# Kernel optimization log

Hardware: AMD Instinct MI355X
Metric: run time of the kernel (lower is better)

Reference implementation:

```python
import jax, jax.numpy as jnp
import numpy as np

NEG = -1000000000.0

def setup_inputs() -> dict:
    key = jax.random.key(0)
    kq, kk, kv, km = jax.random.split(key, 4)
    B, H, S, D = 2, 4, 4096, 64
    q = jax.random.normal(kq, (B, H, S, D), dtype=jnp.float32)
    k = jax.random.normal(kk, (B, H, S, D), dtype=jnp.float32)
    v = jax.random.normal(kv, (B, H, S, D), dtype=jnp.float32)
    mask = jax.random.randint(km, (1, S, S), 0, 2, dtype=jnp.int32)
    return {"q": q, "k": k, "v": v, "mask": mask}

def reference(q, k, v, mask):
    # scores: [B,H,S,S]
    attn = jnp.einsum('bhsd,bhtd->bhst', q, k)
    attn = attn / jnp.sqrt(jnp.asarray(k.shape[-1], dtype=jnp.float32))
    # torch cat/view just broadcasts mask [1,S,S] to [B,H,S,S]
    m = jnp.broadcast_to(mask.astype(bool)[:, None, :, :], attn.shape)
    attn = jnp.where(m, jnp.float32(NEG), attn)
    # NOTE: original module uses nn.Softmax(dim=0) -> softmax over batch axis
    attn = jax.nn.softmax(attn, axis=0)
    out = jnp.einsum('bhst,bhtd->bhsd', attn, v)
    return (out, attn)
```

## Files before the change

kernel.cpp:

```cpp
#include <hip/hip_runtime.h>

#define SDIM 4096
#define DDIM 64
#define HDIM 4
#define OUTN (2 * HDIM * SDIM * DDIM)
#define NTZ 4

typedef short short8 __attribute__((ext_vector_type(8)));
typedef short bh4    __attribute__((ext_vector_type(4)));
typedef float f32x4  __attribute__((ext_vector_type(4)));

__device__ inline short f2bf(float f) {
    unsigned u = __builtin_bit_cast(unsigned, f);
    u = (u + 0x7fffu + ((u >> 16) & 1u)) >> 16;
    return (short)u;
}
__device__ inline float bf2f(short s) {
    unsigned u = ((unsigned)(unsigned short)s) << 16;
    return __builtin_bit_cast(float, u);
}

__device__ inline short* ldsp(short* base, int row, int colshort) {
    int byte = (row << 7) + (colshort << 1);
    byte ^= (row & 7) << 4;
    return (short*)((char*)base + byte);
}

__device__ inline void g2l16(const short* g, short* l) {
    __builtin_amdgcn_global_load_lds(
        (const __attribute__((address_space(1))) unsigned int*)g,
        (__attribute__((address_space(3))) unsigned int*)l, 16, 0, 0);
}

__global__ void pack_mask(const int* __restrict__ mask,
                          unsigned long long* __restrict__ bits) {
    int gid = blockIdx.x * 256 + threadIdx.x;
    int v = (mask[gid] != 0);
    unsigned long long bal = __ballot(v);
    if ((threadIdx.x & 63) == 0) bits[gid >> 6] = bal;
}

__global__ void cvt_bf16(const float* __restrict__ src, short* __restrict__ dst) {
    int gid = blockIdx.x * 256 + threadIdx.x;
    const float* p = src + (size_t)gid * 8;
    f32x4 a = *(const f32x4*)p;
    f32x4 b = *(const f32x4*)(p + 4);
    short8 o;
#pragma unroll
    for (int j = 0; j < 4; ++j) { o[j] = f2bf(a[j]); o[j + 4] = f2bf(b[j]); }
    *(short8*)(dst + (size_t)gid * 8) = o;
}

__global__ void transpose_v(const float* __restrict__ v, short* __restrict__ vt) {
    int gid = blockIdx.x * 256 + threadIdx.x;
    int t8 = gid & (SDIM / 8 - 1);
    int d  = (gid >> 9) & (DDIM - 1);
    int bh = gid >> 15;
    short8 o;
#pragma unroll
    for (int j = 0; j < 8; ++j)
        o[j] = f2bf(v[((size_t)bh * SDIM + t8 * 8 + j) * DDIM + d]);
    *(short8*)(vt + ((size_t)bh * DDIM + d) * SDIM + t8 * 8) = o;
}

__global__ __launch_bounds__(256, 3)
void attn_fused(const short* __restrict__ qg, const short* __restrict__ kg,
                const short* __restrict__ vtg,
                const unsigned long long* __restrict__ mbits,
                float* __restrict__ attng, float* __restrict__ outg,
                float* __restrict__ opart) {
    __shared__ short Ks [2][64 * 64];
    __shared__ short VTs[2][64 * 64];
    __shared__ short Ps [64 * 64];

    const int h   = blockIdx.y;
    const int s0  = blockIdx.x << 6;
    const int tz  = blockIdx.z;
    const int tid = threadIdx.x;
    const int wv  = tid >> 6;
    const int ln  = tid & 63;
    const int l   = ln & 15;
    const int qd  = ln >> 4;

    short8 qf[2][2];
#pragma unroll
    for (int b = 0; b < 2; ++b) {
        const size_t rb = ((size_t)(b * HDIM + h) * SDIM + (s0 + wv * 16 + l)) * DDIM;
#pragma unroll
        for (int kc = 0; kc < 2; ++kc)
            qf[b][kc] = *(const short8*)(qg + rb + kc * 32 + qd * 8);
    }

    f32x4 oacc[2][4];
#pragma unroll
    for (int b = 0; b < 2; ++b)
#pragma unroll
        for (int nd = 0; nd < 4; ++nd)
            oacc[b][nd] = (f32x4){0.f, 0.f, 0.f, 0.f};

    const int ln8 = ln >> 3;
    const int sc_ = (ln & 7) ^ ln8;
    const int mrow0 = s0 + wv * 16 + qd * 4;

    const int tbeg = tz * (SDIM / NTZ);
    for (int t0 = tbeg; t0 < tbeg + SDIM / NTZ; t0 += 64) {
        __syncthreads();
#pragma unroll
        for (int b = 0; b < 2; ++b) {
            const short* kb = kg  + ((size_t)(b * HDIM + h) * SDIM + t0) * DDIM;
            const short* vb = vtg + ((size_t)(b * HDIM + h) * DDIM) * SDIM + t0;
#pragma unroll
            for (int p = 0; p < 2; ++p) {
                int rr = p * 32 + wv * 8 + ln8;
                g2l16(kb + (size_t)rr * DDIM + sc_ * 8, &Ks [b][p * 2048 + wv * 512]);
                g2l16(vb + (size_t)rr * SDIM + sc_ * 8, &VTs[b][p * 2048 + wv * 512]);
            }
        }
        unsigned long long mw[4];
#pragma unroll
        for (int rg = 0; rg < 4; ++rg)
            mw[rg] = mbits[(size_t)(mrow0 + rg) * (SDIM / 64) + (t0 >> 6)];
        __syncthreads();

        f32x4 sc[2][4];
#pragma unroll
        for (int b = 0; b < 2; ++b)
#pragma unroll
            for (int nt = 0; nt < 4; ++nt) {
                f32x4 acc = (f32x4){0.f, 0.f, 0.f, 0.f};
#pragma unroll
                for (int kc = 0; kc < 2; ++kc) {
                    short8 bf = *(const short8*)ldsp(&Ks[b][0], nt * 16 + l, kc * 32 + qd * 8);
                    acc = __builtin_amdgcn_mfma_f32_16x16x32_bf16(qf[b][kc], bf, acc, 0, 0, 0);
                }
                sc[b][nt] = acc;
            }

#pragma unroll
        for (int nt = 0; nt < 4; ++nt)
#pragma unroll
            for (int rg = 0; rg < 4; ++rg) {
                float dd = (sc[0][nt][rg] - sc[1][nt][rg]) * 0.125f;
                bool msk = (mw[rg] >> (nt * 16 + l)) & 1ull;
                float p0 = msk ? 0.5f : __builtin_amdgcn_rcpf(1.f + __expf(-dd));
                int row = wv * 16 + qd * 4 + rg;
                *ldsp(&Ps[0], row, nt * 16 + l) = f2bf(p0);
            }

#pragma unroll
        for (int kc = 0; kc < 2; ++kc) {
            short8 af0 = *(const short8*)ldsp(&Ps[0], wv * 16 + l, kc * 32 + qd * 8);
            short8 af1;
#pragma unroll
            for (int j = 0; j < 8; ++j) af1[j] = f2bf(1.f - bf2f(af0[j]));
#pragma unroll
            for (int nd = 0; nd < 4; ++nd) {
                short8 bf = *(const short8*)ldsp(&VTs[0][0], nd * 16 + l, kc * 32 + qd * 8);
                oacc[0][nd] = __builtin_amdgcn_mfma_f32_16x16x32_bf16(af0, bf, oacc[0][nd], 0, 0, 0);
                short8 bf1 = *(const short8*)ldsp(&VTs[1][0], nd * 16 + l, kc * 32 + qd * 8);
                oacc[1][nd] = __builtin_amdgcn_mfma_f32_16x16x32_bf16(af1, bf1, oacc[1][nd], 0, 0, 0);
            }
        }

        {
            int rr2 = ln >> 4;
            int c2  = ln & 15;
            size_t ab0 = ((size_t)(0 * HDIM + h) * SDIM + s0) * (size_t)SDIM + t0;
            size_t ab1 = ((size_t)(1 * HDIM + h) * SDIM + s0) * (size_t)SDIM + t0;
#pragma unroll
            for (int sub = 0; sub < 4; ++sub) {
                int row = wv * 16 + sub * 4 + rr2;
                bh4 pv = *(const bh4*)ldsp(&Ps[0], row, c2 * 4);
                f32x4 o0, o1;
#pragma unroll
                for (int j = 0; j < 4; ++j) { o0[j] = bf2f(pv[j]); o1[j] = 1.f - o0[j]; }
                __builtin_nontemporal_store(
                    o0, (f32x4*)(attng + ab0 + (size_t)row * SDIM + c2 * 4));
                __builtin_nontemporal_store(
                    o1, (f32x4*)(attng + ab1 + (size_t)row * SDIM + c2 * 4));
            }
        }
    }

    float* dst = (tz == 0) ? outg : (opart + (size_t)(tz - 1) * OUTN);
#pragma unroll
    for (int b = 0; b < 2; ++b)
#pragma unroll
        for (int nd = 0; nd < 4; ++nd)
#pragma unroll
            for (int rg = 0; rg < 4; ++rg) {
                int srow = s0 + wv * 16 + qd * 4 + rg;
                dst[((size_t)(b * HDIM + h) * SDIM + srow) * DDIM + nd * 16 + l] =
                    oacc[b][nd][rg];
            }
}

__global__ void combine(const float* __restrict__ opart, float* __restrict__ outg) {
    int gid = blockIdx.x * 256 + threadIdx.x;
    f32x4 a = *(const f32x4*)(outg + (size_t)gid * 4);
#pragma unroll
    for (int s = 0; s < NTZ - 1; ++s)
        a = a + *(const f32x4*)(opart + (size_t)s * OUTN + (size_t)gid * 4);
    *(f32x4*)(outg + (size_t)gid * 4) = a;
}

extern "C" void kernel_launch(void* const* d_in, const int* in_sizes, int n_in,
                              void* d_out, int out_size, void* d_ws, size_t ws_size,
                              hipStream_t stream) {
    (void)in_sizes; (void)n_in; (void)out_size; (void)ws_size;
    const float* qg  = (const float*)d_in[0];
    const float* kg  = (const float*)d_in[1];
    const float* vg  = (const float*)d_in[2];
    const int*   msk = (const int*)d_in[3];

    float* outg  = (float*)d_out;
    float* attng = outg + (size_t)OUTN;

    char* ws = (char*)d_ws;
    unsigned long long* bits = (unsigned long long*)ws;
    short* qb = (short*)(ws + (size_t) 2 * 1024 * 1024);
    short* kb = (short*)(ws + (size_t) 6 * 1024 * 1024);
    short* vt = (short*)(ws + (size_t)10 * 1024 * 1024);
    float* op = (float*)(ws + (size_t)14 * 1024 * 1024);

    pack_mask  <<<dim3(SDIM * SDIM / 256), dim3(256), 0, stream>>>(msk, bits);
    cvt_bf16   <<<dim3(OUTN / (8 * 256)), dim3(256), 0, stream>>>(qg, qb);
    cvt_bf16   <<<dim3(OUTN / (8 * 256)), dim3(256), 0, stream>>>(kg, kb);
    transpose_v<<<dim3(OUTN / (8 * 256)), dim3(256), 0, stream>>>(vg, vt);
    attn_fused <<<dim3(SDIM / 64, HDIM, NTZ), dim3(256), 0, stream>>>(
        qb, kb, vt, bits, attng, outg, op);
    combine    <<<dim3(OUTN / (4 * 256)), dim3(256), 0, stream>>>(op, outg);
}
```

Before: 217.9 us.

## Compute transposed score tiles and store attention straight from registers in fp32

The QK^T MFMA now takes K as the A operand, so each lane holds four consecutive key columns of one query row. The attention probabilities can then be written to global memory directly from registers as f32x4 stores, with no round trip through the LDS Ps buffer. The mask bit layout is transposed to match, so each lane loads one 64-bit word per tile. The key-dimension split drops from 4 to 2, which lowers the partial-output traffic in combine, and launch bounds drop to 2 blocks per CU. The trade-off is fewer blocks in flight, and the per-lane attention stores are less coalesced, each row being split into 16-byte pieces per lane.

```diff
diff --git a/kernel.cpp b/kernel.cpp
--- a/kernel.cpp
+++ b/kernel.cpp
@@ -4,7 +4,6 @@
 #define DDIM 64
 #define HDIM 4
 #define OUTN (2 * HDIM * SDIM * DDIM)
-#define NTZ 4
 
 typedef short short8 __attribute__((ext_vector_type(8)));
 typedef short bh4    __attribute__((ext_vector_type(4)));
@@ -37,7 +36,11 @@
     int gid = blockIdx.x * 256 + threadIdx.x;
     int v = (mask[gid] != 0);
     unsigned long long bal = __ballot(v);
-    if ((threadIdx.x & 63) == 0) bits[gid >> 6] = bal;
+    if ((threadIdx.x & 63) == 0) {
+        int row = gid >> 12;
+        int tch = (gid & (SDIM - 1)) >> 6;
+        bits[(size_t)tch * SDIM + row] = bal;
+    }
 }
 
 __global__ void cvt_bf16(const float* __restrict__ src, short* __restrict__ dst) {
@@ -63,7 +66,7 @@
     *(short8*)(vt + ((size_t)bh * DDIM + d) * SDIM + t8 * 8) = o;
 }
 
-__global__ __launch_bounds__(256, 3)
+__global__ __launch_bounds__(256, 2)
 void attn_fused(const short* __restrict__ qg, const short* __restrict__ kg,
                 const short* __restrict__ vtg,
                 const unsigned long long* __restrict__ mbits,
@@ -100,10 +103,10 @@
 
     const int ln8 = ln >> 3;
     const int sc_ = (ln & 7) ^ ln8;
-    const int mrow0 = s0 + wv * 16 + qd * 4;
-
-    const int tbeg = tz * (SDIM / NTZ);
-    for (int t0 = tbeg; t0 < tbeg + SDIM / NTZ; t0 += 64) {
+    const int mrow = s0 + wv * 16 + l;
+
+    const int tbeg = tz * (SDIM / 2);
+    for (int t0 = tbeg; t0 < tbeg + SDIM / 2; t0 += 64) {
         __syncthreads();
 #pragma unroll
         for (int b = 0; b < 2; ++b) {
@@ -116,10 +119,7 @@
                 g2l16(vb + (size_t)rr * SDIM + sc_ * 8, &VTs[b][p * 2048 + wv * 512]);
             }
         }
-        unsigned long long mw[4];
-#pragma unroll
-        for (int rg = 0; rg < 4; ++rg)
-            mw[rg] = mbits[(size_t)(mrow0 + rg) * (SDIM / 64) + (t0 >> 6)];
+        unsigned long long mw = mbits[(size_t)(t0 >> 6) * SDIM + mrow];
         __syncthreads();
 
         f32x4 sc[2][4];
@@ -130,22 +130,39 @@
                 f32x4 acc = (f32x4){0.f, 0.f, 0.f, 0.f};
 #pragma unroll
                 for (int kc = 0; kc < 2; ++kc) {
-                    short8 bf = *(const short8*)ldsp(&Ks[b][0], nt * 16 + l, kc * 32 + qd * 8);
-                    acc = __builtin_amdgcn_mfma_f32_16x16x32_bf16(qf[b][kc], bf, acc, 0, 0, 0);
+                    short8 kf = *(const short8*)ldsp(&Ks[b][0], nt * 16 + l, kc * 32 + qd * 8);
+                    acc = __builtin_amdgcn_mfma_f32_16x16x32_bf16(kf, qf[b][kc], acc, 0, 0, 0);
                 }
                 sc[b][nt] = acc;
             }
 
-#pragma unroll
-        for (int nt = 0; nt < 4; ++nt)
+        f32x4 p0[4];
+#pragma unroll
+        for (int nt = 0; nt < 4; ++nt) {
 #pragma unroll
             for (int rg = 0; rg < 4; ++rg) {
                 float dd = (sc[0][nt][rg] - sc[1][nt][rg]) * 0.125f;
-                bool msk = (mw[rg] >> (nt * 16 + l)) & 1ull;
-                float p0 = msk ? 0.5f : __builtin_amdgcn_rcpf(1.f + __expf(-dd));
-                int row = wv * 16 + qd * 4 + rg;
-                *ldsp(&Ps[0], row, nt * 16 + l) = f2bf(p0);
-            }
+                bool msk = (mw >> (nt * 16 + qd * 4 + rg)) & 1ull;
+                p0[nt][rg] = msk ? 0.5f : __builtin_amdgcn_rcpf(1.f + __expf(-dd));
+            }
+            bh4 pb;
+#pragma unroll
+            for (int rg = 0; rg < 4; ++rg) pb[rg] = f2bf(p0[nt][rg]);
+            *(bh4*)ldsp(&Ps[0], wv * 16 + l, nt * 16 + qd * 4) = pb;
+        }
+
+        {
+            float* d0 = attng + ((size_t)h * SDIM + mrow) * (size_t)SDIM + t0 + qd * 4;
+            float* d1 = d0 + (size_t)HDIM * SDIM * SDIM;
+#pragma unroll
+            for (int nt = 0; nt < 4; ++nt) {
+                __builtin_nontemporal_store(p0[nt], (f32x4*)(d0 + nt * 16));
+                f32x4 p1;
+#pragma unroll
+                for (int j = 0; j < 4; ++j) p1[j] = 1.f - p0[nt][j];
+                __builtin_nontemporal_store(p1, (f32x4*)(d1 + nt * 16));
+            }
+        }
 
 #pragma unroll
         for (int kc = 0; kc < 2; ++kc) {
@@ -155,34 +172,15 @@
             for (int j = 0; j < 8; ++j) af1[j] = f2bf(1.f - bf2f(af0[j]));
 #pragma unroll
             for (int nd = 0; nd < 4; ++nd) {
-                short8 bf = *(const short8*)ldsp(&VTs[0][0], nd * 16 + l, kc * 32 + qd * 8);
-                oacc[0][nd] = __builtin_amdgcn_mfma_f32_16x16x32_bf16(af0, bf, oacc[0][nd], 0, 0, 0);
+                short8 bf0 = *(const short8*)ldsp(&VTs[0][0], nd * 16 + l, kc * 32 + qd * 8);
+                oacc[0][nd] = __builtin_amdgcn_mfma_f32_16x16x32_bf16(af0, bf0, oacc[0][nd], 0, 0, 0);
                 short8 bf1 = *(const short8*)ldsp(&VTs[1][0], nd * 16 + l, kc * 32 + qd * 8);
                 oacc[1][nd] = __builtin_amdgcn_mfma_f32_16x16x32_bf16(af1, bf1, oacc[1][nd], 0, 0, 0);
             }
         }
-
-        {
-            int rr2 = ln >> 4;
-            int c2  = ln & 15;
-            size_t ab0 = ((size_t)(0 * HDIM + h) * SDIM + s0) * (size_t)SDIM + t0;
-            size_t ab1 = ((size_t)(1 * HDIM + h) * SDIM + s0) * (size_t)SDIM + t0;
-#pragma unroll
-            for (int sub = 0; sub < 4; ++sub) {
-                int row = wv * 16 + sub * 4 + rr2;
-                bh4 pv = *(const bh4*)ldsp(&Ps[0], row, c2 * 4);
-                f32x4 o0, o1;
-#pragma unroll
-                for (int j = 0; j < 4; ++j) { o0[j] = bf2f(pv[j]); o1[j] = 1.f - o0[j]; }
-                __builtin_nontemporal_store(
-                    o0, (f32x4*)(attng + ab0 + (size_t)row * SDIM + c2 * 4));
-                __builtin_nontemporal_store(
-                    o1, (f32x4*)(attng + ab1 + (size_t)row * SDIM + c2 * 4));
-            }
-        }
     }
 
-    float* dst = (tz == 0) ? outg : (opart + (size_t)(tz - 1) * OUTN);
+    float* dst = (tz == 0) ? outg : opart;
 #pragma unroll
     for (int b = 0; b < 2; ++b)
 #pragma unroll
@@ -198,10 +196,8 @@
 __global__ void combine(const float* __restrict__ opart, float* __restrict__ outg) {
     int gid = blockIdx.x * 256 + threadIdx.x;
     f32x4 a = *(const f32x4*)(outg + (size_t)gid * 4);
-#pragma unroll
-    for (int s = 0; s < NTZ - 1; ++s)
-        a = a + *(const f32x4*)(opart + (size_t)s * OUTN + (size_t)gid * 4);
-    *(f32x4*)(outg + (size_t)gid * 4) = a;
+    f32x4 b = *(const f32x4*)(opart + (size_t)gid * 4);
+    *(f32x4*)(outg + (size_t)gid * 4) = a + b;
 }
 
 extern "C" void kernel_launch(void* const* d_in, const int* in_sizes, int n_in,
@@ -227,7 +223,7 @@
     cvt_bf16   <<<dim3(OUTN / (8 * 256)), dim3(256), 0, stream>>>(qg, qb);
     cvt_bf16   <<<dim3(OUTN / (8 * 256)), dim3(256), 0, stream>>>(kg, kb);
     transpose_v<<<dim3(OUTN / (8 * 256)), dim3(256), 0, stream>>>(vg, vt);
-    attn_fused <<<dim3(SDIM / 64, HDIM, NTZ), dim3(256), 0, stream>>>(
+    attn_fused <<<dim3(SDIM / 64, HDIM, 2), dim3(256), 0, stream>>>(
         qb, kb, vt, bits, attng, outg, op);
     combine    <<<dim3(OUTN / (4 * 256)), dim3(256), 0, stream>>>(op, outg);
 }
```

New measurement: 284.6 us. +30.6%, slower.
